# Kernel optimization log

Hardware: AMD Instinct MI355X
Metric: run time of the kernel (lower is better)

## Reference

```python
import jax, jax.numpy as jnp
import numpy as np

N_NODES = 200000
N_EDGES = 3200000
NUM_FEATURES = 165
HIDDEN = 128
NUM_CLASSES = 2
K = 3  # Chebyshev order for both convs


def setup_inputs() -> dict:
    key = jax.random.key(0)
    k1, k2, k3, k4, k5 = jax.random.split(key, 5)
    x = jax.random.normal(k1, (N_NODES, NUM_FEATURES), dtype=jnp.float32)
    edge_index = jax.random.randint(k2, (2, N_EDGES), 0, N_NODES, dtype=jnp.int64)
    # ChebConv params: K stacked [in, out] weight matrices + bias (Glorot-ish scale)
    W1 = jax.random.normal(k3, (K, NUM_FEATURES, HIDDEN), dtype=jnp.float32) / np.sqrt(NUM_FEATURES)
    b1 = jnp.zeros((HIDDEN,), dtype=jnp.float32)
    W2 = jax.random.normal(k4, (K, HIDDEN, NUM_CLASSES), dtype=jnp.float32) / np.sqrt(HIDDEN)
    b2 = jnp.zeros((NUM_CLASSES,), dtype=jnp.float32)
    return {"x": x, "edge_index": edge_index, "W1": W1, "b1": b1, "W2": W2, "b2": b2}


def _cheb_conv(x, edge_index, W, b):
    """PyG ChebConv with normalization='sym', lambda_max=2.0.
    Scaled Laplacian L_hat = 2L/lambda_max - I = -D^{-1/2} A D^{-1/2}.
    """
    n = x.shape[0]
    row, col = edge_index[0], edge_index[1]
    deg = jax.ops.segment_sum(jnp.ones(row.shape, x.dtype), row, num_segments=n)
    dis = jnp.where(deg > 0, jax.lax.rsqrt(jnp.maximum(deg, 1.0)), 0.0)
    norm = -dis[row] * dis[col]  # [E] edge weights of L_hat (diag entries are 0)

    def prop(h):  # h: [N, F] -> L_hat @ h via gather-multiply-scatter
        return jax.ops.segment_sum(norm[:, None] * h[col], row, num_segments=n)

    Tx0 = x
    out = Tx0 @ W[0]
    if W.shape[0] > 1:
        Tx1 = prop(Tx0)
        out = out + Tx1 @ W[1]
        for k in range(2, W.shape[0]):
            Tx2 = 2.0 * prop(Tx1) - Tx0
            out = out + Tx2 @ W[k]
            Tx0, Tx1 = Tx1, Tx2
    return out + b


def reference(x, edge_index, W1, b1, W2, b2):
    h = jax.nn.relu(_cheb_conv(x, edge_index, W1, b1))
    # F.dropout(training=self.training): identity in eval mode (deterministic reference)
    out = _cheb_conv(h, edge_index, W2, b2)
    return out
```

## Files before the change

kernel.cpp:

```cpp
#include <hip/hip_runtime.h>
#include <hip/hip_bf16.h>
#include <stdint.h>

#define NF 165
#define NH 128
#define KP 192
#define NCOLS 384
#define BSH 8
#define BROWS 256
#define BCAP 6144
#define NSUB 8
#define BSUBCAP 768
#define CPAD 16

typedef __attribute__((ext_vector_type(8))) short bf16x8;
typedef __attribute__((ext_vector_type(4))) float f32x4;


__device__ __forceinline__ unsigned short f2bf(float f) {
    unsigned int u = __builtin_bit_cast(unsigned int, f);
    u = (u + 0x7FFFu + ((u >> 16) & 1u)) >> 16;
    return (unsigned short)u;
}
__device__ __forceinline__ float bf2f_lo(unsigned int v) {
    return __builtin_bit_cast(float, v << 16);
}
__device__ __forceinline__ float bf2f_hi(unsigned int v) {
    return __builtin_bit_cast(float, v & 0xFFFF0000u);
}

#define ACC8(acc, v)                                                   \
    {                                                                  \
        unsigned _vv[4] = {(v).x, (v).y, (v).z, (v).w};                \
        _Pragma("unroll") for (int _j = 0; _j < 4; ++_j) {             \
            acc[2 * _j] += bf2f_lo(_vv[_j]);                           \
            acc[2 * _j + 1] += bf2f_hi(_vv[_j]);                       \
        }                                                              \
    }


__global__ __launch_bounds__(256) void k_bucket(
        const int* __restrict__ erow, const int* __restrict__ ecol,
        int* __restrict__ bcur, unsigned int* __restrict__ bkt, int E) {
    int e = blockIdx.x * 256 + threadIdx.x;
    if (e >= E) return;
    int x = blockIdx.x & (NSUB - 1);
    int r = __builtin_nontemporal_load(erow + e);
    int c = __builtin_nontemporal_load(ecol + e);
    int sub = (r >> BSH) * NSUB + x;
    int pos = atomicAdd(&bcur[sub * CPAD], 1);
    if (pos < BSUBCAP)
        bkt[(size_t)sub * BSUBCAP + pos] =
            ((unsigned)(r & (BROWS - 1)) << 18) | (unsigned)c;
}

__global__ __launch_bounds__(256) void k_hist(
        const int* __restrict__ bcur, const unsigned int* __restrict__ bkt,
        int* __restrict__ cnt, float* __restrict__ dis, int N) {
    __shared__ int h[BROWS];
    int b = blockIdx.x;
    int t = threadIdx.x;
    h[t] = 0;
    __syncthreads();
#pragma unroll
    for (int x = 0; x < NSUB; ++x) {
        int sub = b * NSUB + x;
        int nb = bcur[sub * CPAD];
        if (nb > BSUBCAP) nb = BSUBCAP;
        const unsigned int* src = bkt + (size_t)sub * BSUBCAP;
        for (int i = t; i < nb; i += 256)
            atomicAdd(&h[__builtin_nontemporal_load(src + i) >> 18], 1);
    }
    __syncthreads();
    int base = b << BSH;
    if (base + t < N) {
        int d = h[t];
        cnt[base + t] = d;
        dis[base + t] = (d > 0) ? rsqrtf((float)d) : 0.0f;
    }
}

__global__ __launch_bounds__(256) void k_scan1(
        const int* __restrict__ cnt, int* __restrict__ off,
        int* __restrict__ bsum, int N) {
    __shared__ int sh[256];
    int t = threadIdx.x;
    int base = blockIdx.x * 1024 + t * 4;
    int v0 = (base + 0 < N) ? cnt[base + 0] : 0;
    int v1 = (base + 1 < N) ? cnt[base + 1] : 0;
    int v2 = (base + 2 < N) ? cnt[base + 2] : 0;
    int v3 = (base + 3 < N) ? cnt[base + 3] : 0;
    int tsum = v0 + v1 + v2 + v3;
    sh[t] = tsum;
    __syncthreads();
#pragma unroll
    for (int ofs = 1; ofs < 256; ofs <<= 1) {
        int x = (t >= ofs) ? sh[t - ofs] : 0;
        __syncthreads();
        sh[t] += x;
        __syncthreads();
    }
    int excl = sh[t] - tsum;
    if (t == 255) bsum[blockIdx.x] = sh[t];
    if (base + 0 < N) off[base + 0] = excl;
    excl += v0;
    if (base + 1 < N) off[base + 1] = excl;
    excl += v1;
    if (base + 2 < N) off[base + 2] = excl;
    excl += v2;
    if (base + 3 < N) off[base + 3] = excl;
}

__global__ __launch_bounds__(256) void k_scan2(int* __restrict__ bsum, int NB) {
    __shared__ int sh[256];
    int t = threadIdx.x;
    int v = (t < NB) ? bsum[t] : 0;
    sh[t] = v;
    __syncthreads();
#pragma unroll
    for (int ofs = 1; ofs < 256; ofs <<= 1) {
        int x = (t >= ofs) ? sh[t - ofs] : 0;
        __syncthreads();
        sh[t] += x;
        __syncthreads();
    }
    if (t < NB) bsum[t] = sh[t] - v;
}

__global__ __launch_bounds__(256) void k_scan3(
        int* __restrict__ off, const int* __restrict__ bsum, int N, int E) {
    int i = blockIdx.x * 256 + threadIdx.x;
    if (i >= N) return;
    off[i] = off[i] + bsum[i >> 10];
    if (i == 0) off[N] = E;
}

__global__ __launch_bounds__(256) void k_emit(
        const int* __restrict__ bcur, const unsigned int* __restrict__ bkt,
        const int* __restrict__ off, int* __restrict__ scol, int N) {
    __shared__ unsigned colbuf[BCAP];
    __shared__ int rowoff[BROWS + 1];
    __shared__ int cursor[BROWS];

    int b = blockIdx.x;
    int base = b << BSH;
    int nrows = N - base;
    if (nrows > BROWS) nrows = BROWS;
    int t = threadIdx.x;

    for (int i = t; i <= nrows; i += 256) rowoff[i] = off[base + i];
    if (t < BROWS) cursor[t] = 0;
    __syncthreads();

    int regionStart = rowoff[0];
    int total = rowoff[nrows] - regionStart;

#pragma unroll
    for (int x = 0; x < NSUB; ++x) {
        int sub = b * NSUB + x;
        int nb = bcur[sub * CPAD];
        if (nb > BSUBCAP) nb = BSUBCAP;
        const unsigned int* src = bkt + (size_t)sub * BSUBCAP;
        for (int i = t; i < nb; i += 256) {
            unsigned v = __builtin_nontemporal_load(src + i);
            int rl = v >> 18;
            unsigned c = v & 0x3FFFFu;
            int pos = (rowoff[rl] - regionStart) + atomicAdd(&cursor[rl], 1);
            if (pos < BCAP) colbuf[pos] = c;
        }
    }
    __syncthreads();

    for (int i = t; i < total; i += 256) scol[regionStart + i] = (int)colbuf[i];
}


__global__ __launch_bounds__(256) void k_xb(
        const float* __restrict__ x, unsigned short* __restrict__ xb, int N) {
    int gid = blockIdx.x * 256 + threadIdx.x;
    if (gid >= N * (KP / 8)) return;
    int row = gid / (KP / 8);
    int k0 = (gid % (KP / 8)) * 8;
    unsigned short v[8];
#pragma unroll
    for (int i = 0; i < 8; ++i) {
        int k = k0 + i;
        v[i] = (k < NF) ? f2bf(x[(size_t)row * NF + k]) : (unsigned short)0;
    }
    uint4 pk;
    pk.x = (unsigned)v[0] | ((unsigned)v[1] << 16);
    pk.y = (unsigned)v[2] | ((unsigned)v[3] << 16);
    pk.z = (unsigned)v[4] | ((unsigned)v[5] << 16);
    pk.w = (unsigned)v[6] | ((unsigned)v[7] << 16);
    *(uint4*)(xb + (size_t)row * KP + k0) = pk;
}

__global__ __launch_bounds__(256) void k_wbt(
        const float* __restrict__ W1, unsigned short* __restrict__ wbt) {
    int gid = blockIdx.x * 256 + threadIdx.x;
    if (gid >= NCOLS * (KP / 8)) return;
    int col = gid / (KP / 8);
    int k0 = (gid % (KP / 8)) * 8;
    int cc = col & 127;
    unsigned short v[8];
#pragma unroll
    for (int i = 0; i < 8; ++i) {
        int k = k0 + i;
        float f = 0.0f;
        if (k < NF) {
            if (col < 128)      f = W1[k * 128 + cc] - W1[42240 + k * 128 + cc];
            else if (col < 256) f = W1[21120 + k * 128 + cc];
            else                f = W1[42240 + k * 128 + cc];
        }
        v[i] = f2bf(f);
    }
    uint4 pk;
    pk.x = (unsigned)v[0] | ((unsigned)v[1] << 16);
    pk.y = (unsigned)v[2] | ((unsigned)v[3] << 16);
    pk.z = (unsigned)v[4] | ((unsigned)v[5] << 16);
    pk.w = (unsigned)v[6] | ((unsigned)v[7] << 16);
    *(uint4*)(wbt + (size_t)col * KP + k0) = pk;
}

__global__ __launch_bounds__(256) void k_wc2t(const float* __restrict__ W2,
                                              float* __restrict__ Wc2t) {
    int gid = blockIdx.x * 256 + threadIdx.x;
    if (gid >= 8 * 128) return;
    int t = gid >> 7;
    int k = gid & 127;
    float v = 0.0f;
    if (t < 2)      v = W2[k * 2 + t] - W2[512 + k * 2 + t];
    else if (t < 4) v = W2[256 + k * 2 + (t - 2)];
    else if (t < 6) v = W2[512 + k * 2 + (t - 4)];
    Wc2t[gid] = v;
}

__global__ __launch_bounds__(256) void k_gemm1_mfma(
        const unsigned short* __restrict__ xb, const unsigned short* __restrict__ wbt,
        const float* __restrict__ dis,
        unsigned int* __restrict__ ub, unsigned int* __restrict__ sA,
        unsigned int* __restrict__ wb, int N, int P) {
    int xcd = blockIdx.x & 7;
    int wrk = blockIdx.x >> 3;
    int p = xcd + 8 * (wrk / 3);
    int g = wrk - 3 * (wrk / 3);
    if (p >= P) return;

    __shared__ unsigned short As[128][40];
    __shared__ unsigned short Bs[128][40];

    int tid = threadIdx.x;
    int w = tid >> 6;
    int lane = tid & 63;
    int l15 = lane & 15;
    int l16 = lane >> 4;
    int brow = p * 128;
    int gcol = g * 128;

    int sr = tid >> 1;
    int sk = (tid & 1) * 16;

    f32x4 acc[2][8] = {};

    for (int kc = 0; kc < 6; ++kc) {
        int k0 = kc * 32;
        uint4 va0 = {0, 0, 0, 0}, va1 = {0, 0, 0, 0};
        if (brow + sr < N) {
            const unsigned short* asrc = xb + (size_t)(brow + sr) * KP + k0 + sk;
            va0 = *(const uint4*)asrc;
            va1 = *(const uint4*)(asrc + 8);
        }
        const unsigned short* bsrc = wbt + (size_t)(gcol + sr) * KP + k0 + sk;
        uint4 vb0 = *(const uint4*)bsrc;
        uint4 vb1 = *(const uint4*)(bsrc + 8);
        __syncthreads();
        *(uint4*)&As[sr][sk] = va0;
        *(uint4*)&As[sr][sk + 8] = va1;
        *(uint4*)&Bs[sr][sk] = vb0;
        *(uint4*)&Bs[sr][sk + 8] = vb1;
        __syncthreads();

        bf16x8 a[2], b[8];
#pragma unroll
        for (int m = 0; m < 2; ++m)
            a[m] = *(const bf16x8*)&As[w * 32 + m * 16 + l15][l16 * 8];
#pragma unroll
        for (int n = 0; n < 8; ++n)
            b[n] = *(const bf16x8*)&Bs[n * 16 + l15][l16 * 8];
#pragma unroll
        for (int m = 0; m < 2; ++m)
#pragma unroll
            for (int n = 0; n < 8; ++n)
                acc[m][n] = __builtin_amdgcn_mfma_f32_16x16x32_bf16(
                    a[m], b[n], acc[m][n], 0, 0, 0);
    }

    unsigned int* dst = (g == 0) ? ub : (g == 1) ? sA : wb;
#pragma unroll
    for (int m = 0; m < 2; ++m) {
#pragma unroll
        for (int reg = 0; reg < 4; ++reg) {
            int row = brow + w * 32 + m * 16 + l16 * 4 + reg;
            if (row >= N) continue;
            float sc = (g == 0) ? 1.0f : dis[row];
#pragma unroll
            for (int n = 0; n < 4; ++n) {
                int c = n * 16 + l15;
                float lo = sc * acc[m][n][reg];
                float hi = sc * acc[m][n + 4][reg];
                dst[(size_t)row * 64 + c] =
                    (unsigned)f2bf(lo) | ((unsigned)f2bf(hi) << 16);
            }
        }
    }
}


__global__ __launch_bounds__(256) void k_prop_b2b(
        const int* __restrict__ off, const int* __restrict__ scol,
        const unsigned int* __restrict__ srcb, const unsigned int* __restrict__ addb,
        const float* __restrict__ dis, unsigned int* __restrict__ dstb, int N) {
    int wid = (blockIdx.x * 256 + threadIdx.x) >> 6;
    int lane = threadIdx.x & 63;
    int g = lane >> 4, q = lane & 15;
    int r = wid * 4 + g;
    if (r >= N) return;
    int e = off[r], end = off[r + 1];
    const uint4* src4 = (const uint4*)srcb;
    float a[8] = {}, b[8] = {};
    for (; e + 4 <= end; e += 4) {
        int c0 = scol[e], c1 = scol[e + 1], c2 = scol[e + 2], c3 = scol[e + 3];
        uint4 v0 = src4[(size_t)c0 * 16 + q];
        uint4 v1 = src4[(size_t)c1 * 16 + q];
        uint4 v2 = src4[(size_t)c2 * 16 + q];
        uint4 v3 = src4[(size_t)c3 * 16 + q];
        ACC8(a, v0);
        ACC8(b, v1);
        ACC8(a, v2);
        ACC8(b, v3);
    }
    for (; e < end; ++e) {
        int c0 = scol[e];
        uint4 v0 = src4[(size_t)c0 * 16 + q];
        ACC8(a, v0);
    }
    float d = dis[r];
    float m2 = -2.0f * d * d;
    uint4 ad = ((const uint4*)addb)[(size_t)r * 16 + q];
    unsigned adp[4] = {ad.x, ad.y, ad.z, ad.w};
    uint4 o;
    unsigned* op = (unsigned*)&o;
#pragma unroll
    for (int j = 0; j < 4; ++j) {
        float lo = bf2f_lo(adp[j]) + m2 * (a[2 * j] + b[2 * j]);
        float hi = bf2f_hi(adp[j]) + m2 * (a[2 * j + 1] + b[2 * j + 1]);
        op[j] = (unsigned)f2bf(lo) | ((unsigned)f2bf(hi) << 16);
    }
    ((uint4*)dstb)[(size_t)r * 16 + q] = o;
}

__global__ __launch_bounds__(256) void k_prop_b2f_gemm2(
        const int* __restrict__ off, const int* __restrict__ scol,
        const unsigned int* __restrict__ srcb, const unsigned int* __restrict__ addb,
        const float* __restrict__ dis, const float* __restrict__ b1,
        const float* __restrict__ Wc2t, const float* __restrict__ b2,
        float* __restrict__ out, float* __restrict__ s2, float* __restrict__ w2,
        int N) {
    __shared__ float Ws[8 * 128];
    int tid = threadIdx.x;
    for (int idx = tid; idx < 8 * 128; idx += 256) Ws[idx] = Wc2t[idx];
    __syncthreads();

    int wid = (blockIdx.x * 256 + tid) >> 6;
    int lane = tid & 63;
    int g = lane >> 4, q = lane & 15;
    int r = wid * 4 + g;
    if (r >= N) return;

    float blo[4], bhi[4];
#pragma unroll
    for (int j = 0; j < 4; ++j) {
        blo[j] = b1[q * 4 + j];
        bhi[j] = b1[q * 4 + j + 64];
    }

    int e = off[r], end = off[r + 1];
    const uint4* src4 = (const uint4*)srcb;
    float a[8] = {}, b[8] = {};
    for (; e + 4 <= end; e += 4) {
        int c0 = scol[e], c1 = scol[e + 1], c2 = scol[e + 2], c3 = scol[e + 3];
        uint4 v0 = src4[(size_t)c0 * 16 + q];
        uint4 v1 = src4[(size_t)c1 * 16 + q];
        uint4 v2 = src4[(size_t)c2 * 16 + q];
        uint4 v3 = src4[(size_t)c3 * 16 + q];
        ACC8(a, v0);
        ACC8(b, v1);
        ACC8(a, v2);
        ACC8(b, v3);
    }
    for (; e < end; ++e) {
        int c0 = scol[e];
        uint4 v0 = src4[(size_t)c0 * 16 + q];
        ACC8(a, v0);
    }
    float m1 = -dis[r];
    uint4 ad = ((const uint4*)addb)[(size_t)r * 16 + q];
    unsigned adp[4] = {ad.x, ad.y, ad.z, ad.w};
    float acc[6] = {};
#pragma unroll
    for (int j = 0; j < 4; ++j) {
        int c = q * 4 + j;
        float lo = fmaxf(bf2f_lo(adp[j]) + m1 * (a[2 * j] + b[2 * j]) + blo[j], 0.0f);
        float hi = fmaxf(bf2f_hi(adp[j]) + m1 * (a[2 * j + 1] + b[2 * j + 1]) + bhi[j], 0.0f);
#pragma unroll
        for (int t = 0; t < 6; ++t)
            acc[t] += lo * Ws[t * 128 + c] + hi * Ws[t * 128 + c + 64];
    }
#pragma unroll
    for (int ofs = 8; ofs; ofs >>= 1) {
#pragma unroll
        for (int t = 0; t < 6; ++t)
            acc[t] += __shfl_xor(acc[t], ofs);
    }
    if (q == 0) {
        float d = dis[r];
        out[(size_t)r * 2 + 0] = acc[0] + b2[0];
        out[(size_t)r * 2 + 1] = acc[1] + b2[1];
        s2[(size_t)r * 2 + 0] = d * acc[2];
        s2[(size_t)r * 2 + 1] = d * acc[3];
        w2[(size_t)r * 2 + 0] = d * acc[4];
        w2[(size_t)r * 2 + 1] = d * acc[5];
    }
}

__global__ __launch_bounds__(256) void k_prop2_csr(
        const int* __restrict__ off, const int* __restrict__ scol,
        const float* __restrict__ src, const float* __restrict__ add,
        const float* __restrict__ dis, float* __restrict__ dst,
        int sq, int N) {
    int r = blockIdx.x * 256 + threadIdx.x;
    if (r >= N) return;
    int e0 = off[r], e1 = off[r + 1];
    float a0 = 0.0f, a1 = 0.0f, b0 = 0.0f, b1v = 0.0f;
    int e = e0;
    for (; e + 2 <= e1; e += 2) {
        int c0 = scol[e], c1 = scol[e + 1];
        float2 v0 = *(const float2*)(src + (size_t)c0 * 2);
        float2 v1 = *(const float2*)(src + (size_t)c1 * 2);
        a0 += v0.x; a1 += v0.y;
        b0 += v1.x; b1v += v1.y;
    }
    if (e < e1) {
        int c0 = scol[e];
        float2 v0 = *(const float2*)(src + (size_t)c0 * 2);
        a0 += v0.x; a1 += v0.y;
    }
    a0 += b0; a1 += b1v;
    float d = dis[r];
    float m = sq ? (-2.0f * d * d) : (-d);
    float2 ad = *(const float2*)(add + (size_t)r * 2);
    float2 o = {ad.x + m * a0, ad.y + m * a1};
    *(float2*)(dst + (size_t)r * 2) = o;
}

extern "C" void kernel_launch(void* const* d_in, const int* in_sizes, int n_in,
                              void* d_out, int out_size, void* d_ws, size_t ws_size,
                              hipStream_t stream) {
    const float* x   = (const float*)d_in[0];
    const int* eidx  = (const int*)d_in[1];
    const float* W1  = (const float*)d_in[2];
    const float* b1  = (const float*)d_in[3];
    const float* W2  = (const float*)d_in[4];
    const float* b2  = (const float*)d_in[5];
    float* out       = (float*)d_out;

    int N = in_sizes[0] / NF;
    int E = in_sizes[1] / 2;
    const int* erow = eidx;
    const int* ecol = eidx + E;
    int NBK = (N + BROWS - 1) >> BSH;

    char* p = (char*)d_ws;
    auto alloc = [&](size_t bytes) {
        char* q = p;
        p += (bytes + 255) & ~(size_t)255;
        return q;
    };
    unsigned int* ub = (unsigned int*)alloc((size_t)N * 64 * 4);
    unsigned int* sA = (unsigned int*)alloc((size_t)N * 64 * 4);
    unsigned int* wb = (unsigned int*)alloc((size_t)N * 64 * 4);
    unsigned int* sb = (unsigned int*)alloc((size_t)N * 64 * 4);
    unsigned short* xb  = (unsigned short*)alloc((size_t)N * KP * 2);
    unsigned short* wbt = (unsigned short*)alloc((size_t)NCOLS * KP * 2);
    float* dis  = (float*)alloc((size_t)N * 4);
    int* cnt    = (int*)alloc((size_t)N * 4);
    int* off    = (int*)alloc((size_t)(N + 1) * 4);
    int* bsum   = (int*)alloc((size_t)256 * 4);
    int* bcur   = (int*)alloc((size_t)NBK * NSUB * CPAD * 4);
    unsigned int* bkt = (unsigned int*)alloc((size_t)NBK * NSUB * BSUBCAP * 4);
    int* scol   = (int*)alloc((size_t)E * 4);
    float* Wc2t = (float*)alloc((size_t)8 * 128 * 4);
    float* s2   = (float*)alloc((size_t)N * 2 * 4);
    float* w2   = (float*)alloc((size_t)N * 2 * 4);

    hipMemsetAsync(bcur, 0, (size_t)NBK * NSUB * CPAD * 4, stream);

    int gE = (E + 255) / 256;
    int gN = (N + 255) / 256;
    int NB = (N + 1023) / 1024;

    k_xb<<<(N * (KP / 8) + 255) / 256, 256, 0, stream>>>(x, xb, N);
    k_wbt<<<(NCOLS * (KP / 8) + 255) / 256, 256, 0, stream>>>(W1, wbt);
    k_wc2t<<<4, 256, 0, stream>>>(W2, Wc2t);

    k_bucket<<<gE, 256, 0, stream>>>(erow, ecol, bcur, bkt, E);
    k_hist<<<NBK, 256, 0, stream>>>(bcur, bkt, cnt, dis, N);
    k_scan1<<<NB, 256, 0, stream>>>(cnt, off, bsum, N);
    k_scan2<<<1, 256, 0, stream>>>(bsum, NB);
    k_scan3<<<gN, 256, 0, stream>>>(off, bsum, N, E);
    k_emit<<<NBK, 256, 0, stream>>>(bcur, bkt, off, scol, N);

    int P = (N + 127) / 128;
    int wPerX = 3 * ((P + 7) / 8);
    k_gemm1_mfma<<<8 * wPerX, 256, 0, stream>>>(xb, wbt, dis, ub, sA, wb, N, P);

    int nw4 = (N + 3) / 4;
    int gP4 = (nw4 * 64 + 255) / 256;
    k_prop_b2b<<<gP4, 256, 0, stream>>>(off, scol, wb, sA, dis, sb, N);
    k_prop_b2f_gemm2<<<gP4, 256, 0, stream>>>(off, scol, sb, ub, dis, b1,
                                              Wc2t, b2, out, s2, w2, N);

    k_prop2_csr<<<gN, 256, 0, stream>>>(off, scol, w2, s2, dis, s2, 1, N);
    k_prop2_csr<<<gN, 256, 0, stream>>>(off, scol, s2, out, dis, out, 0, N);
}
```

Before: 633.5 us.

## Stage edge bucketing in shared memory with block-local counting sort

The bucketing kernel now has each block take a tile of 8192 edges, build a shared-memory histogram over row buckets, scan it, and reserve space in each global sub-bucket with a single atomic per bucket. Edges are then scattered into a shared staging buffer sorted by bucket and written out contiguously. This replaces one global atomic per edge and scattered writes with far fewer global atomics and more coalesced stores. In exchange each edge's row is read twice and the kernel uses about 56KB of LDS, which lowers occupancy.

```diff
diff --git a/kernel.cpp b/kernel.cpp
--- a/kernel.cpp
+++ b/kernel.cpp
@@ -12,6 +12,8 @@
 #define NSUB 8
 #define BSUBCAP 768
 #define CPAD 16
+#define TILE 8192
+#define NBKMAX 1024
 
 typedef __attribute__((ext_vector_type(8))) short bf16x8;
 typedef __attribute__((ext_vector_type(4))) float f32x4;
@@ -42,16 +44,73 @@
 __global__ __launch_bounds__(256) void k_bucket(
         const int* __restrict__ erow, const int* __restrict__ ecol,
         int* __restrict__ bcur, unsigned int* __restrict__ bkt, int E) {
-    int e = blockIdx.x * 256 + threadIdx.x;
-    if (e >= E) return;
+    __shared__ int hist[NBKMAX];
+    __shared__ int basex[NBKMAX];
+    __shared__ int gbase[NBKMAX];
+    __shared__ int cur[NBKMAX];
+    __shared__ int scanbuf[256];
+    __shared__ unsigned stage[TILE];
+    __shared__ unsigned short bof[TILE];
+
+    int t = threadIdx.x;
     int x = blockIdx.x & (NSUB - 1);
-    int r = __builtin_nontemporal_load(erow + e);
-    int c = __builtin_nontemporal_load(ecol + e);
-    int sub = (r >> BSH) * NSUB + x;
-    int pos = atomicAdd(&bcur[sub * CPAD], 1);
-    if (pos < BSUBCAP)
-        bkt[(size_t)sub * BSUBCAP + pos] =
-            ((unsigned)(r & (BROWS - 1)) << 18) | (unsigned)c;
+    int e0 = blockIdx.x * TILE;
+    int cnt = E - e0;
+    if (cnt > TILE) cnt = TILE;
+    if (cnt <= 0) return;
+
+    for (int i = t; i < NBKMAX; i += 256) { hist[i] = 0; cur[i] = 0; }
+    __syncthreads();
+
+    for (int i = t; i < cnt; i += 256) {
+        int r = __builtin_nontemporal_load(erow + e0 + i);
+        atomicAdd(&hist[r >> BSH], 1);
+    }
+    __syncthreads();
+
+    int b0 = 4 * t;
+    int h0 = hist[b0], h1 = hist[b0 + 1], h2 = hist[b0 + 2], h3 = hist[b0 + 3];
+    int tsum = h0 + h1 + h2 + h3;
+    scanbuf[t] = tsum;
+    __syncthreads();
+#pragma unroll
+    for (int ofs = 1; ofs < 256; ofs <<= 1) {
+        int v = (t >= ofs) ? scanbuf[t - ofs] : 0;
+        __syncthreads();
+        scanbuf[t] += v;
+        __syncthreads();
+    }
+    int excl = scanbuf[t] - tsum;
+    basex[b0] = excl;
+    basex[b0 + 1] = excl + h0;
+    basex[b0 + 2] = excl + h0 + h1;
+    basex[b0 + 3] = excl + h0 + h1 + h2;
+    int hb[4] = {h0, h1, h2, h3};
+#pragma unroll
+    for (int j = 0; j < 4; ++j) {
+        int b = b0 + j;
+        if (hb[j] > 0)
+            gbase[b] = atomicAdd(&bcur[(b * NSUB + x) * CPAD], hb[j]);
+    }
+    __syncthreads();
+
+    for (int i = t; i < cnt; i += 256) {
+        int r = __builtin_nontemporal_load(erow + e0 + i);
+        int c = __builtin_nontemporal_load(ecol + e0 + i);
+        int b = r >> BSH;
+        int rk = atomicAdd(&cur[b], 1);
+        int pos = basex[b] + rk;
+        stage[pos] = ((unsigned)(r & (BROWS - 1)) << 18) | (unsigned)c;
+        bof[pos] = (unsigned short)b;
+    }
+    __syncthreads();
+
+    for (int i = t; i < cnt; i += 256) {
+        int b = bof[i];
+        int slot = gbase[b] + (i - basex[b]);
+        if (slot < BSUBCAP)
+            bkt[(size_t)(b * NSUB + x) * BSUBCAP + slot] = stage[i];
+    }
 }
 
 __global__ __launch_bounds__(256) void k_hist(
@@ -505,7 +564,6 @@
 
     hipMemsetAsync(bcur, 0, (size_t)NBK * NSUB * CPAD * 4, stream);
 
-    int gE = (E + 255) / 256;
     int gN = (N + 255) / 256;
     int NB = (N + 1023) / 1024;
 
@@ -513,7 +571,8 @@
     k_wbt<<<(NCOLS * (KP / 8) + 255) / 256, 256, 0, stream>>>(W1, wbt);
     k_wc2t<<<4, 256, 0, stream>>>(W2, Wc2t);
 
-    k_bucket<<<gE, 256, 0, stream>>>(erow, ecol, bcur, bkt, E);
+    int gT = (E + TILE - 1) / TILE;
+    k_bucket<<<gT, 256, 0, stream>>>(erow, ecol, bcur, bkt, E);
     k_hist<<<NBK, 256, 0, stream>>>(bcur, bkt, cnt, dis, N);
     k_scan1<<<NB, 256, 0, stream>>>(cnt, off, bsum, N);
     k_scan2<<<1, 256, 0, stream>>>(bsum, NB);
```

New measurement: 547.0 us. 13.7% less time.
